# Kernel tuning notes

Hardware: AMD Instinct MI355X
Metric: run time of the kernel (lower is better)

The kernel has to match this reference:

```python
import jax, jax.numpy as jnp
import numpy as np

D_Z, D_Y, N, N_SAMPLE = 512, 32, 2048, 128
JITTER = 0.0001


def setup_inputs() -> dict:
    key = jax.random.key(0)
    k1, k2, k3, k4, k5 = jax.random.split(key, 5)
    d_total = D_Z + N * D_Y
    return {
        "m": jax.random.normal(k1, (d_total,), jnp.float32),
        "Lz": jax.random.normal(k2, (D_Z, D_Z), jnp.float32),
        "Ly_blocks": jax.random.normal(k3, (N, D_Y, D_Y), jnp.float32),
        "Lyz": jax.random.normal(k4, (N * D_Y, D_Z), jnp.float32),
        "eps": jax.random.normal(k5, (N_SAMPLE, d_total), jnp.float32),
    }


def reference(m, Lz, Ly_blocks, Lyz, eps):
    # L_dense (block lower-triangular) is never materialized; we compute
    # z = m + eps @ L_dense.T block-wise. L_dense = [[tril(Lz), 0], [Lyz, blkdiag(tril(Ly_n))]] + jitter*I.
    dt = Lz.dtype
    Lz_t = jnp.tril(Lz) + JITTER * jnp.eye(D_Z, dtype=dt)
    Ly = jnp.tril(Ly_blocks) + JITTER * jnp.eye(D_Y, dtype=dt)  # [N, d_y, d_y]

    eps_z = eps[:, :D_Z]                          # [S, d_z]
    eps_y = eps[:, D_Z:].reshape(-1, N, D_Y)      # [S, N, d_y]

    z_z = m[:D_Z] + eps_z @ Lz_t.T                # [S, d_z]
    cross = eps_z @ Lyz.T                         # [S, N*d_y]
    diag = jnp.einsum("snj,nij->sni", eps_y, Ly).reshape(-1, N * D_Y)
    z_y = m[D_Z:] + cross + diag                  # [S, N*d_y]
    return jnp.concatenate([z_z, z_y], axis=1)
```

## Files before the change

kernel.cpp:

```cpp
#include <hip/hip_runtime.h>

#define DZ 512
#define DT 66048
#define NSTRIP 1032
#define SV_JITTER 1e-4f
#define BIGD 0x3FFFFFFF

typedef __attribute__((ext_vector_type(8))) short bf8;
typedef __attribute__((ext_vector_type(4))) float f4;

__device__ __forceinline__ short f2bf(float f) {
  unsigned u = __builtin_bit_cast(unsigned, f);
  return (short)((u + 0x7FFFu + ((u >> 16) & 1u)) >> 16);
}

__device__ __forceinline__ bf8 cvt8(float4 a, float4 b) {
  bf8 r = { f2bf(a.x), f2bf(a.y), f2bf(a.z), f2bf(a.w),
            f2bf(b.x), f2bf(b.y), f2bf(b.z), f2bf(b.w) };
  return r;
}

__device__ __forceinline__ bf8 cvt8_tril(float4 x, float4 y, int kbase, int diag) {
  float v[8] = {x.x, x.y, x.z, x.w, y.x, y.y, y.z, y.w};
  bf8 r;
  #pragma unroll
  for (int t = 0; t < 8; ++t) {
    int k = kbase + t;
    float val = (k < diag) ? v[t] : ((k == diag) ? v[t] + SV_JITTER : 0.f);
    r[t] = f2bf(val);
  }
  return r;
}

__global__ __launch_bounds__(512, 2)
void sv_kernel(const float* __restrict__ mv, const float* __restrict__ Lz,
               const float* __restrict__ Ly, const float* __restrict__ Lyz,
               const float* __restrict__ eps, float* __restrict__ out) {
  __shared__ short Afrag[128 * 512];

  const int tid = threadIdx.x;
  const int lane = tid & 63;
  const int wv = tid >> 6;
  const int lcol = lane & 15;
  const int q = lane >> 4;
  const int mh = wv & 1;
  const int cg = wv >> 1;
  const int rbase = 4 * mh;

  {
    const int slot = tid & 63;
    const int r0 = (tid >> 6) * 16;
    #pragma unroll 4
    for (int i = 0; i < 16; ++i) {
      const int r = r0 + i;
      const float* p = eps + (size_t)(16 * (r & 7) + (slot & 15)) * DT +
                       (r >> 3) * 32 + (slot >> 4) * 8;
      float4 x = *(const float4*)p;
      float4 y = *(const float4*)(p + 4);
      *(bf8*)&Afrag[r * 512 + slot * 8] = cvt8(x, y);
    }
  }
  __syncthreads();

  for (int j = 0; j < 5; ++j) {
    const int s = blockIdx.x + 256 * j;
    if (s >= NSTRIP) break;
    const bool is_z = (s < 8);
    const int c0 = s * 64 + 16 * cg;
    const int colL = c0 + lcol;
    const int bdiag = is_z ? colL : BIGD;
    const float* bptr = is_z ? (Lz + (size_t)colL * DZ)
                             : (Lyz + (size_t)(colL - DZ) * DZ);

    f4 acc[4];
    #pragma unroll
    for (int mi = 0; mi < 4; ++mi) acc[mi] = f4{0.f, 0.f, 0.f, 0.f};

    float4 bx0, by0, bx1, by1, bx2, by2, bx3, by3;
    bf8 a0[4], a1[4];

    auto loadB = [&](int kk, float4& x, float4& y) {
      const float* p = bptr + kk * 32 + 8 * q;
      x = *(const float4*)p;
      y = *(const float4*)(p + 4);
    };
    auto loadA = [&](int kk, bf8* a) {
      #pragma unroll
      for (int mi = 0; mi < 4; ++mi)
        a[mi] = *(const bf8*)&Afrag[(kk * 8 + rbase + mi) * 512 + lane * 8];
    };
    auto domfma = [&](const bf8* a, bf8 bf) {
      #pragma unroll
      for (int mi = 0; mi < 4; ++mi)
        acc[mi] = __builtin_amdgcn_mfma_f32_16x16x32_bf16(a[mi], bf, acc[mi], 0, 0, 0);
    };

    loadB(0, bx0, by0); loadB(1, bx1, by1);
    loadB(2, bx2, by2); loadB(3, bx3, by3);
    loadA(0, a0); loadA(1, a1);

    int kk = 0;
    #pragma unroll 1
    for (int kt = 0; kt < 3; ++kt, kk += 4) {
      { bf8 bf = cvt8_tril(bx0, by0, kk * 32 + 8 * q, bdiag);
        domfma(a0, bf); loadB(kk + 4, bx0, by0); loadA(kk + 2, a0); }
      { bf8 bf = cvt8_tril(bx1, by1, (kk + 1) * 32 + 8 * q, bdiag);
        domfma(a1, bf); loadB(kk + 5, bx1, by1); loadA(kk + 3, a1); }
      { bf8 bf = cvt8_tril(bx2, by2, (kk + 2) * 32 + 8 * q, bdiag);
        domfma(a0, bf); loadB(kk + 6, bx2, by2); loadA(kk + 4, a0); }
      { bf8 bf = cvt8_tril(bx3, by3, (kk + 3) * 32 + 8 * q, bdiag);
        domfma(a1, bf); loadB(kk + 7, bx3, by3); loadA(kk + 5, a1); }
    }

    float4 dax[4], day[4], dbx, dby;
    int dI = 0;
    if (!is_z) {
      const int nb = (c0 - DZ) >> 5;
      dI = (c0 - DZ) & 31;
      const float* pb = Ly + ((size_t)nb * 32 + dI + lcol) * 32 + 8 * q;
      dbx = *(const float4*)pb; dby = *(const float4*)(pb + 4);
      #pragma unroll
      for (int mi = 0; mi < 4; ++mi) {
        const float* pa =
            eps + (size_t)(64 * mh + 16 * mi + lcol) * DT + DZ + nb * 32 + 8 * q;
        dax[mi] = *(const float4*)pa; day[mi] = *(const float4*)(pa + 4);
      }
    }

    { bf8 bf = cvt8_tril(bx0, by0, 12 * 32 + 8 * q, bdiag);
      domfma(a0, bf); loadA(14, a0); }
    { bf8 bf = cvt8_tril(bx1, by1, 13 * 32 + 8 * q, bdiag);
      domfma(a1, bf); loadA(15, a1); }
    { bf8 bf = cvt8_tril(bx2, by2, 14 * 32 + 8 * q, bdiag); domfma(a0, bf); }
    { bf8 bf = cvt8_tril(bx3, by3, 15 * 32 + 8 * q, bdiag); domfma(a1, bf); }

    if (!is_z) {
      bf8 bf = cvt8_tril(dbx, dby, 8 * q, dI + lcol);
      #pragma unroll
      for (int mi = 0; mi < 4; ++mi) {
        bf8 af = cvt8(dax[mi], day[mi]);
        acc[mi] = __builtin_amdgcn_mfma_f32_16x16x32_bf16(af, bf, acc[mi], 0, 0, 0);
      }
    }

    const float mval = mv[colL];
    #pragma unroll
    for (int mi = 0; mi < 4; ++mi) {
      #pragma unroll
      for (int r = 0; r < 4; ++r) {
        out[(size_t)(64 * mh + 16 * mi + 4 * q + r) * DT + colL] = acc[mi][r] + mval;
      }
    }
  }
}

extern "C" void kernel_launch(void* const* d_in, const int* in_sizes, int n_in,
                              void* d_out, int out_size, void* d_ws, size_t ws_size,
                              hipStream_t stream) {
  const float* m   = (const float*)d_in[0];
  const float* Lz  = (const float*)d_in[1];
  const float* Ly  = (const float*)d_in[2];
  const float* Lyz = (const float*)d_in[3];
  const float* eps = (const float*)d_in[4];
  float* out = (float*)d_out;
  sv_kernel<<<dim3(256), dim3(512), 0, stream>>>(m, Lz, Ly, Lyz, eps, out);
}
```

Before: 63.29 us.

## Give each wave a full 128-row by 16-column tile and template the z path

Each wave now computes all 128 sample rows for one 16-column strip instead of half the rows, so each B fragment (Lz/Lyz row) is loaded and converted once per wave rather than twice. Tiles are distributed per wave across the grid (up to 3 rounds), and a template parameter removes the triangular masking from the Lyz path. This doubles the accumulator and A-fragment register footprint, which may raise register pressure or cause spills under the launch bound of 2 blocks per CU.

Result: faster. 55.12 us (-12.9%).

```diff
diff --git a/kernel.cpp b/kernel.cpp
--- a/kernel.cpp
+++ b/kernel.cpp
@@ -2,9 +2,8 @@
 
 #define DZ 512
 #define DT 66048
-#define NSTRIP 1032
+#define NT 4128
 #define SV_JITTER 1e-4f
-#define BIGD 0x3FFFFFFF
 
 typedef __attribute__((ext_vector_type(8))) short bf8;
 typedef __attribute__((ext_vector_type(4))) float f4;
@@ -32,6 +31,111 @@
   return r;
 }
 
+template <bool IS_Z>
+__device__ __forceinline__ void process_tile(
+    int col0, int lcol, int q, int lane, const short* __restrict__ Afrag,
+    const float* __restrict__ mv, const float* __restrict__ Lz,
+    const float* __restrict__ Ly, const float* __restrict__ Lyz,
+    const float* __restrict__ eps, float* __restrict__ out) {
+  const int colL = col0 + lcol;
+  const float* bptr = IS_Z ? (Lz + (size_t)colL * DZ)
+                           : (Lyz + (size_t)(colL - DZ) * DZ);
+  const int bdiag = colL;
+
+  f4 acc[8];
+  #pragma unroll
+  for (int mi = 0; mi < 8; ++mi) acc[mi] = f4{0.f, 0.f, 0.f, 0.f};
+
+  float4 bx0, by0, bx1, by1, bx2, by2, bx3, by3;
+  bf8 a0[8], a1[8];
+
+  auto loadB = [&](int kk, float4& x, float4& y) {
+    const float* p = bptr + kk * 32 + 8 * q;
+    x = *(const float4*)p;
+    y = *(const float4*)(p + 4);
+  };
+  auto loadA = [&](int kk, bf8* a) {
+    #pragma unroll
+    for (int mi = 0; mi < 8; ++mi)
+      a[mi] = *(const bf8*)&Afrag[(kk * 8 + mi) * 512 + lane * 8];
+  };
+  auto mk = [&](float4 x, float4 y, int kb) {
+    return IS_Z ? cvt8_tril(x, y, kb, bdiag) : cvt8(x, y);
+  };
+  auto domfma = [&](const bf8* a, bf8 bf) {
+    #pragma unroll
+    for (int mi = 0; mi < 8; ++mi)
+      acc[mi] = __builtin_amdgcn_mfma_f32_16x16x32_bf16(a[mi], bf, acc[mi], 0, 0, 0);
+  };
+
+  loadB(0, bx0, by0); loadB(1, bx1, by1);
+  loadB(2, bx2, by2); loadB(3, bx3, by3);
+  loadA(0, a0); loadA(1, a1);
+
+  int kk = 0;
+  #pragma unroll 1
+  for (int kt = 0; kt < 3; ++kt, kk += 4) {
+    { bf8 bf = mk(bx0, by0, kk * 32 + 8 * q);
+      domfma(a0, bf); loadB(kk + 4, bx0, by0); loadA(kk + 2, a0); }
+    { bf8 bf = mk(bx1, by1, (kk + 1) * 32 + 8 * q);
+      domfma(a1, bf); loadB(kk + 5, bx1, by1); loadA(kk + 3, a1); }
+    { bf8 bf = mk(bx2, by2, (kk + 2) * 32 + 8 * q);
+      domfma(a0, bf); loadB(kk + 6, bx2, by2); loadA(kk + 4, a0); }
+    { bf8 bf = mk(bx3, by3, (kk + 3) * 32 + 8 * q);
+      domfma(a1, bf); loadB(kk + 7, bx3, by3); loadA(kk + 5, a1); }
+  }
+
+  float4 dbx{}, dby{};
+  int nb = 0, dI = 0;
+  if (!IS_Z) {
+    nb = (col0 - DZ) >> 5;
+    dI = (col0 - DZ) & 31;
+    const float* pb = Ly + ((size_t)nb * 32 + dI + lcol) * 32 + 8 * q;
+    dbx = *(const float4*)pb; dby = *(const float4*)(pb + 4);
+  }
+
+  { bf8 bf = mk(bx0, by0, 12 * 32 + 8 * q); domfma(a0, bf); loadA(14, a0); }
+  { bf8 bf = mk(bx1, by1, 13 * 32 + 8 * q); domfma(a1, bf); loadA(15, a1); }
+  { bf8 bf = mk(bx2, by2, 14 * 32 + 8 * q); domfma(a0, bf); }
+  { bf8 bf = mk(bx3, by3, 15 * 32 + 8 * q); domfma(a1, bf); }
+
+  if (!IS_Z) {
+    const bf8 dbf = cvt8_tril(dbx, dby, 8 * q, dI + lcol);
+    const float* abase = eps + (size_t)lcol * DT + DZ + nb * 32 + 8 * q;
+    float4 rx[4], ry[4];
+    #pragma unroll
+    for (int mi = 0; mi < 4; ++mi) {
+      const float* pa = abase + (size_t)mi * 16 * DT;
+      rx[mi] = *(const float4*)pa; ry[mi] = *(const float4*)(pa + 4);
+    }
+    float4 sx[4], sy[4];
+    #pragma unroll
+    for (int mi = 0; mi < 4; ++mi) {
+      const float* pa = abase + (size_t)(mi + 4) * 16 * DT;
+      sx[mi] = *(const float4*)pa; sy[mi] = *(const float4*)(pa + 4);
+    }
+    #pragma unroll
+    for (int mi = 0; mi < 4; ++mi) {
+      bf8 af = cvt8(rx[mi], ry[mi]);
+      acc[mi] = __builtin_amdgcn_mfma_f32_16x16x32_bf16(af, dbf, acc[mi], 0, 0, 0);
+    }
+    #pragma unroll
+    for (int mi = 0; mi < 4; ++mi) {
+      bf8 af = cvt8(sx[mi], sy[mi]);
+      acc[mi + 4] = __builtin_amdgcn_mfma_f32_16x16x32_bf16(af, dbf, acc[mi + 4], 0, 0, 0);
+    }
+  }
+
+  const float mval = mv[colL];
+  #pragma unroll
+  for (int mi = 0; mi < 8; ++mi) {
+    #pragma unroll
+    for (int r = 0; r < 4; ++r) {
+      out[(size_t)(16 * mi + 4 * q + r) * DT + colL] = acc[mi][r] + mval;
+    }
+  }
+}
+
 __global__ __launch_bounds__(512, 2)
 void sv_kernel(const float* __restrict__ mv, const float* __restrict__ Lz,
                const float* __restrict__ Ly, const float* __restrict__ Lyz,
@@ -43,9 +147,6 @@
   const int wv = tid >> 6;
   const int lcol = lane & 15;
   const int q = lane >> 4;
-  const int mh = wv & 1;
-  const int cg = wv >> 1;
-  const int rbase = 4 * mh;
 
   {
     const int slot = tid & 63;
@@ -62,95 +163,15 @@
   }
   __syncthreads();
 
-  for (int j = 0; j < 5; ++j) {
-    const int s = blockIdx.x + 256 * j;
-    if (s >= NSTRIP) break;
-    const bool is_z = (s < 8);
-    const int c0 = s * 64 + 16 * cg;
-    const int colL = c0 + lcol;
-    const int bdiag = is_z ? colL : BIGD;
-    const float* bptr = is_z ? (Lz + (size_t)colL * DZ)
-                             : (Lyz + (size_t)(colL - DZ) * DZ);
-
-    f4 acc[4];
-    #pragma unroll
-    for (int mi = 0; mi < 4; ++mi) acc[mi] = f4{0.f, 0.f, 0.f, 0.f};
-
-    float4 bx0, by0, bx1, by1, bx2, by2, bx3, by3;
-    bf8 a0[4], a1[4];
-
-    auto loadB = [&](int kk, float4& x, float4& y) {
-      const float* p = bptr + kk * 32 + 8 * q;
-      x = *(const float4*)p;
-      y = *(const float4*)(p + 4);
-    };
-    auto loadA = [&](int kk, bf8* a) {
-      #pragma unroll
-      for (int mi = 0; mi < 4; ++mi)
-        a[mi] = *(const bf8*)&Afrag[(kk * 8 + rbase + mi) * 512 + lane * 8];
-    };
-    auto domfma = [&](const bf8* a, bf8 bf) {
-      #pragma unroll
-      for (int mi = 0; mi < 4; ++mi)
-        acc[mi] = __builtin_amdgcn_mfma_f32_16x16x32_bf16(a[mi], bf, acc[mi], 0, 0, 0);
-    };
-
-    loadB(0, bx0, by0); loadB(1, bx1, by1);
-    loadB(2, bx2, by2); loadB(3, bx3, by3);
-    loadA(0, a0); loadA(1, a1);
-
-    int kk = 0;
-    #pragma unroll 1
-    for (int kt = 0; kt < 3; ++kt, kk += 4) {
-      { bf8 bf = cvt8_tril(bx0, by0, kk * 32 + 8 * q, bdiag);
-        domfma(a0, bf); loadB(kk + 4, bx0, by0); loadA(kk + 2, a0); }
-      { bf8 bf = cvt8_tril(bx1, by1, (kk + 1) * 32 + 8 * q, bdiag);
-        domfma(a1, bf); loadB(kk + 5, bx1, by1); loadA(kk + 3, a1); }
-      { bf8 bf = cvt8_tril(bx2, by2, (kk + 2) * 32 + 8 * q, bdiag);
-        domfma(a0, bf); loadB(kk + 6, bx2, by2); loadA(kk + 4, a0); }
-      { bf8 bf = cvt8_tril(bx3, by3, (kk + 3) * 32 + 8 * q, bdiag);
-        domfma(a1, bf); loadB(kk + 7, bx3, by3); loadA(kk + 5, a1); }
-    }
-
-    float4 dax[4], day[4], dbx, dby;
-    int dI = 0;
-    if (!is_z) {
-      const int nb = (c0 - DZ) >> 5;
-      dI = (c0 - DZ) & 31;
-      const float* pb = Ly + ((size_t)nb * 32 + dI + lcol) * 32 + 8 * q;
-      dbx = *(const float4*)pb; dby = *(const float4*)(pb + 4);
-      #pragma unroll
-      for (int mi = 0; mi < 4; ++mi) {
-        const float* pa =
-            eps + (size_t)(64 * mh + 16 * mi + lcol) * DT + DZ + nb * 32 + 8 * q;
-        dax[mi] = *(const float4*)pa; day[mi] = *(const float4*)(pa + 4);
-      }
-    }
-
-    { bf8 bf = cvt8_tril(bx0, by0, 12 * 32 + 8 * q, bdiag);
-      domfma(a0, bf); loadA(14, a0); }
-    { bf8 bf = cvt8_tril(bx1, by1, 13 * 32 + 8 * q, bdiag);
-      domfma(a1, bf); loadA(15, a1); }
-    { bf8 bf = cvt8_tril(bx2, by2, 14 * 32 + 8 * q, bdiag); domfma(a0, bf); }
-    { bf8 bf = cvt8_tril(bx3, by3, 15 * 32 + 8 * q, bdiag); domfma(a1, bf); }
-
-    if (!is_z) {
-      bf8 bf = cvt8_tril(dbx, dby, 8 * q, dI + lcol);
-      #pragma unroll
-      for (int mi = 0; mi < 4; ++mi) {
-        bf8 af = cvt8(dax[mi], day[mi]);
-        acc[mi] = __builtin_amdgcn_mfma_f32_16x16x32_bf16(af, bf, acc[mi], 0, 0, 0);
-      }
-    }
-
-    const float mval = mv[colL];
-    #pragma unroll
-    for (int mi = 0; mi < 4; ++mi) {
-      #pragma unroll
-      for (int r = 0; r < 4; ++r) {
-        out[(size_t)(64 * mh + 16 * mi + 4 * q + r) * DT + colL] = acc[mi][r] + mval;
-      }
-    }
+  #pragma unroll 1
+  for (int r = 0; r < 3; ++r) {
+    const int T = r * 2048 + blockIdx.x * 8 + wv;
+    if (T >= NT) break;
+    const int col0 = T * 16;
+    if (col0 < DZ)
+      process_tile<true>(col0, lcol, q, lane, Afrag, mv, Lz, Ly, Lyz, eps, out);
+    else
+      process_tile<false>(col0, lcol, q, lane, Afrag, mv, Lz, Ly, Lyz, eps, out);
   }
 }
 
```
